# Kernel tuning notes

Hardware: AMD Instinct MI355X
Metric: run time of the kernel (lower is better)

Reference implementation:

```python
import jax, jax.numpy as jnp
import numpy as np

N, D_IM, D_CLI = 2048, 1024, 64
EPS = 1e-12  # F.normalize eps


def setup_inputs() -> dict:
    key = jax.random.key(0)
    k1, k2, k3, k4 = jax.random.split(key, 4)
    phi_im = jax.random.normal(k1, (N, D_IM), dtype=jnp.float32)
    phi_cli = jax.random.normal(k2, (N, D_CLI), dtype=jnp.float32)
    t = jax.random.randint(k3, (N, 2), 0, 3, dtype=jnp.int64)
    traumatic = jax.random.randint(k4, (N,), 0, 2, dtype=jnp.int64)
    return {"phi_im": phi_im, "phi_cli": phi_cli, "t": t, "traumatic": traumatic}


def _l2norm(x):
    n = jnp.sqrt(jnp.sum(x * x, axis=1, keepdims=True))
    return x / jnp.maximum(n, EPS)


def _pair_block(S, ma, mb):
    # S: [N,N] full cosine similarity; ma, mb: [N] bool group masks.
    valid = ma[:, None] & mb[None, :]
    mat = jnp.where(valid, S, 0.0)            # scatter-into-zero matrix semantics
    masked = jnp.where(valid, S, jnp.inf)     # masked argmin = nearest (least similar) pair
    flat = jnp.argmin(masked.reshape(-1))
    i = flat // S.shape[1]
    j = flat % S.shape[1]
    return mat, masked.reshape(-1)[flat], jnp.stack([i, j])


def reference(phi_im, phi_cli, t, traumatic):
    im_n = _l2norm(phi_im)
    cli_n = _l2norm(phi_cli)
    # single batched GEMM replaces the per-pair python loops
    S_im = im_n @ im_n.T    # [N,N]
    S_cli = cli_n @ cli_n.T  # [N,N]

    t1 = t[:, 1]
    m0 = (t1 == 0) & (traumatic == 1)
    m1 = t1 == 1
    m2 = t1 == 2

    mats, vals, idxs = [], [], []
    for S in (S_im, S_cli):
        for (ma, mb) in ((m0, m1), (m0, m2), (m1, m2)):
            mat, v, ij = _pair_block(S, ma, mb)
            mats.append(mat)
            vals.append(v)
            idxs.append(ij)
    sims = jnp.stack(mats)           # [6, N, N]: im_01, im_02, im_12, cli_01, cli_02, cli_12
    min_vals = jnp.stack(vals)       # [6]
    min_idx = jnp.stack(idxs)        # [6, 2]
    return sims, min_vals, min_idx
```

## Files before the change

kernel.cpp:

```cpp
#include <hip/hip_runtime.h>
#include <stdint.h>

#define NROW 2048
#define D_IM 1024
#define D_CLI 64
#define EPSF 1e-12f
#define NN ((size_t)NROW * (size_t)NROW)
#define GRID_GEMM 800

typedef __attribute__((ext_vector_type(8))) short bf16x8;
typedef __attribute__((ext_vector_type(4))) float f32x4;

#define OFF_PACKED   0
#define OFF_CNT      64
#define OFF_CAT      128
#define OFF_LISTS    8320
#define OFF_POS      32896
#define OFF_COLINFO  41216
#define OFF_INVIM    65792
#define OFF_INVCLI   73984
#define OFF_PIM      82176
#define OFF_PCLI     8470784
#define OFF_SC       8995072

__device__ __forceinline__ unsigned int enc_f32(float x) {
    unsigned int u = __float_as_uint(x);
    return (u & 0x80000000u) ? ~u : (u | 0x80000000u);
}
__device__ __forceinline__ unsigned short bf16rn(float x) {
    unsigned int u = __float_as_uint(x);
    return (unsigned short)((u + 0x7FFFu + ((u >> 16) & 1u)) >> 16);
}
__device__ __forceinline__ float bf16tof(unsigned short h) {
    return __uint_as_float(((unsigned int)h) << 16);
}

__global__ __launch_bounds__(256)
void prepscan_kernel(const float* __restrict__ phi_im,
                     const float* __restrict__ phi_cli,
                     const int* __restrict__ t,
                     const int* __restrict__ traumatic,
                     float* __restrict__ inv_im,
                     float* __restrict__ inv_cli,
                     char* __restrict__ pim,
                     char* __restrict__ pcli,
                     int* __restrict__ cnt,
                     int* __restrict__ catArr,
                     int* __restrict__ lists,
                     int* __restrict__ posIn,
                     unsigned int* __restrict__ colinfo,
                     unsigned long long* __restrict__ packed,
                     float* __restrict__ out) {
    __shared__ unsigned long long shmem[256];
    const int tid = threadIdx.x;

    if (blockIdx.x > NROW) {
        const int row = blockIdx.x - (NROW + 1);
        const int t1 = t[2 * row + 1];
        const int tr = traumatic[row];
        if (t1 == 0 && tr == 1) return;
        float* orow = out + (size_t)row * NROW;
        const f32x4 z4 = (f32x4){0.f, 0.f, 0.f, 0.f};
        __builtin_nontemporal_store(z4, (f32x4*)orow + tid);
        __builtin_nontemporal_store(z4, (f32x4*)orow + tid + 256);
        return;
    }

    if (blockIdx.x == NROW) {
        int cats[8];
        unsigned long long mycnt = 0;
        #pragma unroll
        for (int e = 0; e < 8; e++) {
            int r = tid * 8 + e;
            int t1 = t[2 * r + 1];
            int tr = traumatic[r];
            int c = (t1 == 1) ? 1 : ((t1 == 2) ? 2 : ((tr == 1) ? 0 : 3));
            cats[e] = c;
            catArr[r] = c;
            if (c < 3) mycnt += 1ULL << (21 * c);
        }
        shmem[tid] = mycnt;
        __syncthreads();
        for (int off = 1; off < 256; off <<= 1) {
            unsigned long long v = (tid >= off) ? shmem[tid - off] : 0ULL;
            __syncthreads();
            shmem[tid] += v;
            __syncthreads();
        }
        unsigned long long excl = shmem[tid] - mycnt;
        unsigned long long tot = shmem[255];
        unsigned int loc[3];
        #pragma unroll
        for (int c = 0; c < 3; c++)
            loc[c] = (unsigned int)(excl >> (21 * c)) & 0x1FFFFFu;
        #pragma unroll
        for (int e = 0; e < 8; e++) {
            int r = tid * 8 + e;
            int c = cats[e];
            unsigned int slot = 0xFFFFFFFFu;
            if (c < 3) {
                slot = loc[c]++;
                lists[c * 2048 + slot] = r;
                posIn[r] = (int)slot;
            }
            colinfo[0 * 2048 + r] = (c == 1) ? slot : 0xFFFFFFFFu;
            colinfo[1 * 2048 + r] = (c == 2) ? slot : 0xFFFFFFFFu;
            colinfo[2 * 2048 + r] = (c == 2) ? slot : 0xFFFFFFFFu;
        }
        if (tid == 0) {
            cnt[0] = (int)(tot & 0x1FFFFFu);
            cnt[1] = (int)((tot >> 21) & 0x1FFFFFu);
            cnt[2] = (int)((tot >> 42) & 0x1FFFFFu);
            cnt[3] = 0;
        }
        if (tid < 6) packed[tid] = 0xFFFFFFFFFFFFFFFFULL;
        return;
    }

    float* sred = (float*)shmem;
    const int r = blockIdx.x;

    float4 v = ((const float4*)(phi_im + (size_t)r * D_IM))[tid];
    float a[4] = {v.x, v.y, v.z, v.w};
    unsigned short h4[4], l4[4];
    #pragma unroll
    for (int e = 0; e < 4; e++) {
        h4[e] = bf16rn(a[e]);
        l4[e] = bf16rn(a[e] - bf16tof(h4[e]));
    }
    {
        char* rowb = pim + (size_t)r * 4096 + (tid >> 1) * 32 + (tid & 1) * 8;
        *(ushort4*)rowb = make_ushort4(h4[0], h4[1], h4[2], h4[3]);
        *(ushort4*)(rowb + 16) = make_ushort4(l4[0], l4[1], l4[2], l4[3]);
    }
    sred[tid] = a[0] * a[0] + a[1] * a[1] + a[2] * a[2] + a[3] * a[3];
    __syncthreads();
    for (int off = 128; off > 0; off >>= 1) {
        if (tid < off) sred[tid] += sred[tid + off];
        __syncthreads();
    }
    if (tid == 0) inv_im[r] = 1.0f / fmaxf(sqrtf(sred[0]), EPSF);

    if (tid < 16) {
        float4 c = ((const float4*)(phi_cli + (size_t)r * D_CLI))[tid];
        float b[4] = {c.x, c.y, c.z, c.w};
        unsigned short ch[4], cl[4];
        #pragma unroll
        for (int e = 0; e < 4; e++) {
            ch[e] = bf16rn(b[e]);
            cl[e] = bf16rn(b[e] - bf16tof(ch[e]));
        }
        char* rowb = pcli + (size_t)r * 256 + (tid >> 1) * 32 + (tid & 1) * 8;
        *(ushort4*)rowb = make_ushort4(ch[0], ch[1], ch[2], ch[3]);
        *(ushort4*)(rowb + 16) = make_ushort4(cl[0], cl[1], cl[2], cl[3]);
    }
    if (tid < 64) {
        float c = phi_cli[(size_t)r * D_CLI + tid];
        float cs = c * c;
        #pragma unroll
        for (int off = 32; off > 0; off >>= 1) cs += __shfl_down(cs, off, 64);
        if (tid == 0) inv_cli[r] = 1.0f / fmaxf(sqrtf(cs), EPSF);
    }
}

#define LOAD_SET(s, AH, AL, BH, BL)                                        \
    {                                                                      \
        const int kb_ = (s) * 128;                                         \
        _Pragma("unroll") for (int q = 0; q < 2; q++) {                    \
            AH[q] = *(const bf16x8*)(pX + offA[q] + kb_);                  \
            AL[q] = *(const bf16x8*)(pX + offA[q] + kb_ + 16);             \
            BH[q] = *(const bf16x8*)(pX + offB[q] + kb_);                  \
            BL[q] = *(const bf16x8*)(pX + offB[q] + kb_ + 16);             \
        }                                                                  \
    }
#define MFMA_SET(AH, AL, BH, BL)                                           \
    _Pragma("unroll") for (int lm = 0; lm < 2; lm++)                       \
        _Pragma("unroll") for (int ln = 0; ln < 2; ln++) {                 \
            acc[lm][ln] = __builtin_amdgcn_mfma_f32_16x16x32_bf16(         \
                AH[lm], BH[ln], acc[lm][ln], 0, 0, 0);                     \
            acc[lm][ln] = __builtin_amdgcn_mfma_f32_16x16x32_bf16(         \
                AH[lm], BL[ln], acc[lm][ln], 0, 0, 0);                     \
            acc[lm][ln] = __builtin_amdgcn_mfma_f32_16x16x32_bf16(         \
                AL[lm], BH[ln], acc[lm][ln], 0, 0, 0);                     \
        }

__global__ __launch_bounds__(256, 2)
void gemm_kernel(const char* __restrict__ pim,
                 const char* __restrict__ pcli,
                 const float* __restrict__ inv_im,
                 const float* __restrict__ inv_cli,
                 const int* __restrict__ cnt,
                 const int* __restrict__ lists,
                 const int* __restrict__ catArr,
                 unsigned short* __restrict__ Sc,
                 float* __restrict__ out,
                 unsigned long long* __restrict__ packed) {
    const int tid = threadIdx.x;

    if (blockIdx.x >= GRID_GEMM) {
        const int b = blockIdx.x - GRID_GEMM;
        const int pzf = 1 + (b >> 11);
        const int row = b & 2047;
        const int p = (pzf < 3) ? pzf : pzf - 3;
        const int rowcat = (p == 2) ? 1 : 0;
        if (catArr[row] == rowcat) return;
        float* orow = out + (size_t)pzf * NN + (size_t)row * NROW;
        const f32x4 z4 = (f32x4){0.f, 0.f, 0.f, 0.f};
        __builtin_nontemporal_store(z4, (f32x4*)orow + tid);
        __builtin_nontemporal_store(z4, (f32x4*)orow + tid + 256);
        return;
    }

    __shared__ float sIA[64], sIB[64];
    __shared__ int sRA[64], sRB[64];

    const int n0 = cnt[0], n1 = cnt[1], n2 = cnt[2];
    const int tA = (n0 + 63) >> 6, tB = (n1 + 63) >> 6, tC = (n2 + 63) >> 6;
    const int T0 = tA * tB, T1 = tA * tC, T2 = tB * tC;
    const int tot = T0 + T1 + T2;
    int bid = blockIdx.x;
    if (bid >= 2 * tot) return;
    int z = 0;
    if (bid >= tot) { z = 1; bid -= tot; }
    const size_t s0 = (size_t)(tA << 6) * (tB << 6);
    const size_t s1 = (size_t)(tA << 6) * (tC << 6);
    const size_t s2 = (size_t)(tB << 6) * (tC << 6);
    size_t scoff = z ? (s0 + s1 + s2) : 0;
    int gx, nA, nB, nBpad, pp;
    const int *lA, *lB;
    if (bid < T0)           { pp = 0; gx = tB; nA = n0; nB = n1; lA = lists;        lB = lists + 2048; nBpad = tB << 6; }
    else if (bid < T0 + T1) { bid -= T0;      scoff += s0;      pp = 1; gx = tC; nA = n0; nB = n2; lA = lists;        lB = lists + 4096; nBpad = tC << 6; }
    else                    { bid -= T0 + T1; scoff += s0 + s1; pp = 2; gx = tC; nA = n1; nB = n2; lA = lists + 2048; lB = lists + 4096; nBpad = tC << 6; }
    const int by = bid / gx, bx = bid % gx;
    const int i0 = by << 6, j0 = bx << 6;
    const int pz = z * 3 + pp;

    const char* __restrict__ pX = z ? pcli : pim;
    const float* __restrict__ inv = z ? inv_cli : inv_im;
    const int steps = z ? (D_CLI / 32) : (D_IM / 32);
    const size_t stride = z ? 256 : 4096;
    const int lane = tid & 63;
    const int wid = tid >> 6;
    const int wr = wid >> 1;
    const int wc = wid & 1;

    if (tid < 64) {
        int ia = lA[min(i0 + tid, nA - 1)];
        int ib = lB[min(j0 + tid, nB - 1)];
        sRA[tid] = ia; sRB[tid] = ib;
        sIA[tid] = inv[ia]; sIB[tid] = inv[ib];
    }
    __syncthreads();

    const int mrow = lane & 15;
    const int quad = lane >> 4;
    size_t offA[2], offB[2];
    #pragma unroll
    for (int q = 0; q < 2; q++) {
        offA[q] = (size_t)sRA[(wr * 2 + q) * 16 + mrow] * stride + quad * 32;
        offB[q] = (size_t)sRB[(wc * 2 + q) * 16 + mrow] * stride + quad * 32;
    }

    f32x4 acc[2][2];
    #pragma unroll
    for (int lm = 0; lm < 2; lm++)
        #pragma unroll
        for (int ln = 0; ln < 2; ln++)
            acc[lm][ln] = (f32x4){0.f, 0.f, 0.f, 0.f};

    bf16x8 A0h[2], A0l[2], B0h[2], B0l[2];
    bf16x8 A1h[2], A1l[2], B1h[2], B1l[2];
    LOAD_SET(0, A0h, A0l, B0h, B0l);
    for (int s = 0; s < steps; s += 2) {
        if (s + 1 < steps) LOAD_SET(s + 1, A1h, A1l, B1h, B1l);
        MFMA_SET(A0h, A0l, B0h, B0l);
        if (s + 2 < steps) LOAD_SET(s + 2, A0h, A0l, B0h, B0l);
        if (s + 1 < steps) MFMA_SET(A1h, A1l, B1h, B1l);
    }

    unsigned long long best = 0xFFFFFFFFFFFFFFFFULL;
    #pragma unroll
    for (int lm = 0; lm < 2; lm++)
        #pragma unroll
        for (int ln = 0; ln < 2; ln++) {
            const int cloc = (wc * 2 + ln) * 16 + mrow;
            const float ivb = sIB[cloc];
            const unsigned int jcol = (unsigned int)sRB[cloc];
            #pragma unroll
            for (int rr = 0; rr < 4; rr++) {
                const int rloc = (wr * 2 + lm) * 16 + quad * 4 + rr;
                float sv = acc[lm][ln][rr] * (sIA[rloc] * ivb);
                Sc[scoff + (size_t)(i0 + rloc) * nBpad + (j0 + cloc)] = bf16rn(sv);
                unsigned long long pk =
                    ((unsigned long long)enc_f32(sv) << 32) |
                    ((unsigned int)sRA[rloc] * (unsigned int)NROW + jcol);
                if (pk < best) best = pk;
            }
        }
    #pragma unroll
    for (int off = 32; off > 0; off >>= 1) {
        unsigned long long o = __shfl_down(best, off, 64);
        if (o < best) best = o;
    }
    if (lane == 0) atomicMin(&packed[pz], best);
}

__global__ __launch_bounds__(256)
void writer_kernel(const unsigned short* __restrict__ Sc,
                   const int* __restrict__ cnt,
                   const int* __restrict__ catArr,
                   const int* __restrict__ posIn,
                   const unsigned int* __restrict__ colinfo,
                   float* __restrict__ out,
                   const unsigned long long* __restrict__ packed) {
    const int b = blockIdx.x;
    const int tid = threadIdx.x;
    if (b == 6 * NROW) {
        const int p = tid;
        if (p < 6) {
            unsigned long long pk = packed[p];
            float v;
            unsigned int flat;
            if (pk == 0xFFFFFFFFFFFFFFFFULL) { v = __builtin_huge_valf(); flat = 0u; }
            else {
                unsigned int key = (unsigned int)(pk >> 32);
                flat = (unsigned int)pk;
                unsigned int bits = (key & 0x80000000u) ? (key ^ 0x80000000u) : ~key;
                v = __uint_as_float(bits);
            }
            out[6 * NN + p] = v;
            out[6 * NN + 6 + 2 * p + 0] = (float)(flat >> 11);
            out[6 * NN + 6 + 2 * p + 1] = (float)(flat & 2047u);
        }
        return;
    }
    const int pz = b >> 11;
    const int row = b & 2047;
    const int z = pz / 3, p = pz - 3 * z;

    const int rowcat = (p == 2) ? 1 : 0;
    if (catArr[row] != rowcat) {
        if (pz < 4) return;
        float* orow = out + (size_t)pz * NN + (size_t)row * NROW;
        const f32x4 z4 = (f32x4){0.f, 0.f, 0.f, 0.f};
        __builtin_nontemporal_store(z4, (f32x4*)orow + tid);
        __builtin_nontemporal_store(z4, (f32x4*)orow + tid + 256);
        return;
    }

    float* orow = out + (size_t)pz * NN + (size_t)row * NROW;

    const int n0 = cnt[0], n1 = cnt[1], n2 = cnt[2];
    const int tA = (n0 + 63) >> 6, tB = (n1 + 63) >> 6, tC = (n2 + 63) >> 6;
    const size_t s0 = (size_t)(tA << 6) * (tB << 6);
    const size_t s1 = (size_t)(tA << 6) * (tC << 6);
    const size_t s2 = (size_t)(tB << 6) * (tC << 6);
    size_t scoff = z ? (s0 + s1 + s2) : 0;
    int nBpad;
    if (p == 0)      { nBpad = tB << 6; }
    else if (p == 1) { scoff += s0;      nBpad = tC << 6; }
    else             { scoff += s0 + s1; nBpad = tC << 6; }

    const unsigned short* srow = Sc + scoff + (size_t)posIn[row] * nBpad;
    const uint4* cinfo4 = (const uint4*)(colinfo + p * 2048);

    #pragma unroll
    for (int seg = 0; seg < 2; seg++) {
        const int j4 = tid + seg * 256;
        uint4 inf = cinfo4[j4];
        f32x4 vv;
        vv[0] = (inf.x != 0xFFFFFFFFu) ? bf16tof(srow[inf.x]) : 0.f;
        vv[1] = (inf.y != 0xFFFFFFFFu) ? bf16tof(srow[inf.y]) : 0.f;
        vv[2] = (inf.z != 0xFFFFFFFFu) ? bf16tof(srow[inf.z]) : 0.f;
        vv[3] = (inf.w != 0xFFFFFFFFu) ? bf16tof(srow[inf.w]) : 0.f;
        __builtin_nontemporal_store(vv, (f32x4*)orow + j4);
    }
}

extern "C" void kernel_launch(void* const* d_in, const int* in_sizes, int n_in,
                              void* d_out, int out_size, void* d_ws, size_t ws_size,
                              hipStream_t stream) {
    const float* phi_im = (const float*)d_in[0];
    const float* phi_cli = (const float*)d_in[1];
    const int* t = (const int*)d_in[2];
    const int* traumatic = (const int*)d_in[3];
    float* out = (float*)d_out;

    char* ws = (char*)d_ws;
    unsigned long long* packed = (unsigned long long*)(ws + OFF_PACKED);
    int* cnt = (int*)(ws + OFF_CNT);
    int* catArr = (int*)(ws + OFF_CAT);
    int* lists = (int*)(ws + OFF_LISTS);
    int* posIn = (int*)(ws + OFF_POS);
    unsigned int* colinfo = (unsigned int*)(ws + OFF_COLINFO);
    float* inv_im = (float*)(ws + OFF_INVIM);
    float* inv_cli = (float*)(ws + OFF_INVCLI);
    char* pim = ws + OFF_PIM;
    char* pcli = ws + OFF_PCLI;
    unsigned short* Sc = (unsigned short*)(ws + OFF_SC);

    prepscan_kernel<<<2 * NROW + 1, 256, 0, stream>>>(
        phi_im, phi_cli, t, traumatic, inv_im, inv_cli, pim, pcli,
        cnt, catArr, lists, posIn, colinfo, packed, out);
    gemm_kernel<<<GRID_GEMM + 3 * NROW, 256, 0, stream>>>(
        pim, pcli, inv_im, inv_cli, cnt, lists, catArr, Sc, out, packed);
    writer_kernel<<<6 * NROW + 1, 256, 0, stream>>>(Sc, cnt, catArr, posIn,
                                                    colinfo, out, packed);
}
```

Measured before the change: 190.3 us.

## Stage GEMM operand tiles through LDS with register prefetch and padded row stride

The GEMM previously had every wave load its A/B fragments straight from global memory. Now the block loads each k-slice once with coalesced 16-byte loads, writes it to a double-buffered LDS tile, and the waves read their MFMA fragments from LDS. This is meant to cut redundant global traffic and uncoalesced gathers. The packed image-row stride is padded from 4096 to 4352 bytes to avoid channel or bank conflicts, which shifts the workspace offsets. In exchange it adds four __syncthreads per two k-steps and extra LDS use, which may reduce occupancy.

Measured after the change: 168.0 us. 1.13x faster.

```diff
diff --git a/kernel.cpp b/kernel.cpp
--- a/kernel.cpp
+++ b/kernel.cpp
@@ -7,6 +7,7 @@
 #define EPSF 1e-12f
 #define NN ((size_t)NROW * (size_t)NROW)
 #define GRID_GEMM 800
+#define PIM_STRIDE 4352
 
 typedef __attribute__((ext_vector_type(8))) short bf16x8;
 typedef __attribute__((ext_vector_type(4))) float f32x4;
@@ -20,8 +21,8 @@
 #define OFF_INVIM    65792
 #define OFF_INVCLI   73984
 #define OFF_PIM      82176
-#define OFF_PCLI     8470784
-#define OFF_SC       8995072
+#define OFF_PCLI     8995072
+#define OFF_SC       9519360
 
 __device__ __forceinline__ unsigned int enc_f32(float x) {
     unsigned int u = __float_as_uint(x);
@@ -129,7 +130,7 @@
         l4[e] = bf16rn(a[e] - bf16tof(h4[e]));
     }
     {
-        char* rowb = pim + (size_t)r * 4096 + (tid >> 1) * 32 + (tid & 1) * 8;
+        char* rowb = pim + (size_t)r * PIM_STRIDE + (tid >> 1) * 32 + (tid & 1) * 8;
         *(ushort4*)rowb = make_ushort4(h4[0], h4[1], h4[2], h4[3]);
         *(ushort4*)(rowb + 16) = make_ushort4(l4[0], l4[1], l4[2], l4[3]);
     }
@@ -163,16 +164,6 @@
     }
 }
 
-#define LOAD_SET(s, AH, AL, BH, BL)                                        \
-    {                                                                      \
-        const int kb_ = (s) * 128;                                         \
-        _Pragma("unroll") for (int q = 0; q < 2; q++) {                    \
-            AH[q] = *(const bf16x8*)(pX + offA[q] + kb_);                  \
-            AL[q] = *(const bf16x8*)(pX + offA[q] + kb_ + 16);             \
-            BH[q] = *(const bf16x8*)(pX + offB[q] + kb_);                  \
-            BL[q] = *(const bf16x8*)(pX + offB[q] + kb_ + 16);             \
-        }                                                                  \
-    }
 #define MFMA_SET(AH, AL, BH, BL)                                           \
     _Pragma("unroll") for (int lm = 0; lm < 2; lm++)                       \
         _Pragma("unroll") for (int ln = 0; ln < 2; ln++) {                 \
@@ -183,6 +174,30 @@
             acc[lm][ln] = __builtin_amdgcn_mfma_f32_16x16x32_bf16(         \
                 AL[lm], BH[ln], acc[lm][ln], 0, 0, 0);                     \
         }
+
+#define LOAD_REGS(RA, RB, OFF)                                             \
+    RA[0] = *(const f32x4*)(pX + gA0 + (OFF));                             \
+    RA[1] = *(const f32x4*)(pX + gA1 + (OFF));                             \
+    RB[0] = *(const f32x4*)(pX + gB0 + (OFF));                             \
+    RB[1] = *(const f32x4*)(pX + gB1 + (OFF));
+
+#define STAGE_WRITE(B, RA, RB)                                             \
+    *(f32x4*)(&sT[B][0][my_e][my_r * 16]) = RA[0];                         \
+    *(f32x4*)(&sT[B][0][my_e][(32 + my_r) * 16]) = RA[1];                  \
+    *(f32x4*)(&sT[B][1][my_e][my_r * 16]) = RB[0];                         \
+    *(f32x4*)(&sT[B][1][my_e][(32 + my_r) * 16]) = RB[1];
+
+#define COMPUTE(B)                                                         \
+    {                                                                      \
+        bf16x8 AH[2], AL[2], BH[2], BL[2];                                 \
+        _Pragma("unroll") for (int q = 0; q < 2; q++) {                    \
+            AH[q] = *(const bf16x8*)(&sT[B][0][2 * quad][aoff[q]]);        \
+            AL[q] = *(const bf16x8*)(&sT[B][0][2 * quad + 1][aoff[q]]);    \
+            BH[q] = *(const bf16x8*)(&sT[B][1][2 * quad][boff[q]]);        \
+            BL[q] = *(const bf16x8*)(&sT[B][1][2 * quad + 1][boff[q]]);    \
+        }                                                                  \
+        MFMA_SET(AH, AL, BH, BL)                                           \
+    }
 
 __global__ __launch_bounds__(256, 2)
 void gemm_kernel(const char* __restrict__ pim,
@@ -213,6 +228,7 @@
 
     __shared__ float sIA[64], sIB[64];
     __shared__ int sRA[64], sRB[64];
+    __shared__ __align__(16) char sT[2][2][8][1040];
 
     const int n0 = cnt[0], n1 = cnt[1], n2 = cnt[2];
     const int tA = (n0 + 63) >> 6, tB = (n1 + 63) >> 6, tC = (n2 + 63) >> 6;
@@ -237,8 +253,8 @@
 
     const char* __restrict__ pX = z ? pcli : pim;
     const float* __restrict__ inv = z ? inv_cli : inv_im;
-    const int steps = z ? (D_CLI / 32) : (D_IM / 32);
-    const size_t stride = z ? 256 : 4096;
+    const int nst = z ? (D_CLI / 32) : (D_IM / 32);
+    const size_t stride = z ? 256 : PIM_STRIDE;
     const int lane = tid & 63;
     const int wid = tid >> 6;
     const int wr = wid >> 1;
@@ -254,11 +270,19 @@
 
     const int mrow = lane & 15;
     const int quad = lane >> 4;
-    size_t offA[2], offB[2];
+
+    const int my_e = tid & 7;
+    const int my_r = tid >> 3;
+    const size_t gA0 = (size_t)sRA[my_r] * stride + my_e * 16;
+    const size_t gA1 = (size_t)sRA[32 + my_r] * stride + my_e * 16;
+    const size_t gB0 = (size_t)sRB[my_r] * stride + my_e * 16;
+    const size_t gB1 = (size_t)sRB[32 + my_r] * stride + my_e * 16;
+
+    int aoff[2], boff[2];
     #pragma unroll
     for (int q = 0; q < 2; q++) {
-        offA[q] = (size_t)sRA[(wr * 2 + q) * 16 + mrow] * stride + quad * 32;
-        offB[q] = (size_t)sRB[(wc * 2 + q) * 16 + mrow] * stride + quad * 32;
+        aoff[q] = ((wr * 2 + q) * 16 + mrow) * 16;
+        boff[q] = ((wc * 2 + q) * 16 + mrow) * 16;
     }
 
     f32x4 acc[2][2];
@@ -268,14 +292,22 @@
         for (int ln = 0; ln < 2; ln++)
             acc[lm][ln] = (f32x4){0.f, 0.f, 0.f, 0.f};
 
-    bf16x8 A0h[2], A0l[2], B0h[2], B0l[2];
-    bf16x8 A1h[2], A1l[2], B1h[2], B1l[2];
-    LOAD_SET(0, A0h, A0l, B0h, B0l);
-    for (int s = 0; s < steps; s += 2) {
-        if (s + 1 < steps) LOAD_SET(s + 1, A1h, A1l, B1h, B1l);
-        MFMA_SET(A0h, A0l, B0h, B0l);
-        if (s + 2 < steps) LOAD_SET(s + 2, A0h, A0l, B0h, B0l);
-        if (s + 1 < steps) MFMA_SET(A1h, A1l, B1h, B1l);
+    f32x4 ra0[2], rb0[2], ra1[2], rb1[2];
+    LOAD_REGS(ra0, rb0, 0);
+    LOAD_REGS(ra1, rb1, 128);
+
+    for (int st = 0; st < nst; st += 2) {
+        STAGE_WRITE(0, ra0, rb0);
+        __syncthreads();
+        if (st + 2 < nst) { LOAD_REGS(ra0, rb0, (size_t)(st + 2) * 128); }
+        COMPUTE(0);
+        __syncthreads();
+
+        STAGE_WRITE(1, ra1, rb1);
+        __syncthreads();
+        if (st + 3 < nst) { LOAD_REGS(ra1, rb1, (size_t)(st + 3) * 128); }
+        COMPUTE(1);
+        __syncthreads();
     }
 
     unsigned long long best = 0xFFFFFFFFFFFFFFFFULL;
```
